# Kernel tuning notes

Hardware: AMD Instinct MI355X
Metric: run time of the kernel (lower is better)

The kernel has to match this reference:

```python
import jax, jax.numpy as jnp
import numpy as np
from jax import lax

V, E, H = 10000, 512, 512
B, L, T = 128, 8, 48


def setup_inputs() -> dict:
    key = jax.random.key(0)
    ks = jax.random.split(key, 12)
    s = lambda k, shape: jax.random.normal(k, shape, jnp.float32) * 0.05
    kw_lens = jnp.sort(jax.random.randint(ks[2], (B,), 1, L + 1))[::-1]  # descending, as pack_padded requires
    return {
        "kws": jax.random.randint(ks[0], (B, L), 0, V),
        "poem": jax.random.randint(ks[1], (B, T), 0, V),
        "kw_lens": kw_lens,
        "embedding": s(ks[3], (V, E)),
        "enc_Wih": s(ks[4], (4 * H, E)), "enc_Whh": s(ks[5], (4 * H, H)), "enc_b": s(ks[6], (4 * H,)),
        "dec_Wih": s(ks[7], (4 * H, E)), "dec_Whh": s(ks[8], (4 * H, H)), "dec_b": s(ks[9], (4 * H,)),
        "out_W": s(ks[10], (V, 2 * H)), "out_b": s(ks[11], (V,)),
    }


def _lstm_step(h, c, x, Wih, Whh, b):
    # PyTorch gate order: i, f, g, o
    gates = x @ Wih.T + h @ Whh.T + b  # [B, 4H]
    i, f, g, o = jnp.split(gates, 4, axis=-1)
    c = jax.nn.sigmoid(f) * c + jax.nn.sigmoid(i) * jnp.tanh(g)
    h = jax.nn.sigmoid(o) * jnp.tanh(c)
    return h, c


def reference(kws, poem, kw_lens, embedding, enc_Wih, enc_Whh, enc_b,
              dec_Wih, dec_Whh, dec_b, out_W, out_b):
    bs = kws.shape[0]
    mask = jnp.arange(L)[None, :] < kw_lens[:, None]  # sequence_mask, [B, L]

    # ---- encoder LSTM over keywords (dropout inactive at eval) ----
    kws_emb = embedding[kws]  # [B, L, E]

    def enc_scan(carry, x):
        h, c = carry
        h, c = _lstm_step(h, c, x, enc_Wih, enc_Whh, enc_b)
        return (h, c), (h, c)

    z = jnp.zeros((bs, H), embedding.dtype)
    _, (hs, cs) = lax.scan(enc_scan, (z, z), kws_emb.transpose(1, 0, 2))  # [L, B, H]
    kws_rep = hs.transpose(1, 0, 2) * mask[..., None]  # pad_packed zeros past length
    # pack semantics: final hidden is the state at the last valid timestep
    bidx = jnp.arange(bs)
    h0 = hs[kw_lens - 1, bidx]
    c0 = cs[kw_lens - 1, bidx]

    # ---- greedy per-timestep decode with dot-product attention ----
    neg = jnp.asarray(-1e9, embedding.dtype)

    def dec_scan(carry, tok):
        h, c = carry
        x = embedding[tok]  # [B, E]
        h, c = _lstm_step(h, c, x, dec_Wih, dec_Whh, dec_b)
        scores = jnp.einsum('bh,blh->bl', h, kws_rep)
        attn = jax.nn.softmax(jnp.where(mask, scores, neg), axis=-1)
        ctx = jnp.einsum('bl,blh->bh', attn, kws_rep)
        logits = jnp.concatenate([h, ctx], axis=-1) @ out_W.T + out_b  # [B, V]
        return (h, c), logits

    _, preds = lax.scan(dec_scan, (h0, c0), poem.T)  # [T, B, V]
    return preds.transpose(1, 0, 2)  # [B, T, V]
```

## Files before the change

### kernel.cpp

```cpp
#include <hip/hip_runtime.h>
#include <hip/hip_bf16.h>

typedef __bf16 bf16;
typedef __attribute__((ext_vector_type(8))) __bf16 bf16x8;
typedef __attribute__((ext_vector_type(4))) __bf16 bf16x4;
typedef __attribute__((ext_vector_type(4))) float f32x4;

#define B_ 128
#define L_ 8
#define T_ 48
#define V_ 10000
#define NBLK_REC 32
#define NBLK_TOT 240
#define NW (NBLK_TOT - NBLK_REC)

__device__ __forceinline__ float sigf(float x) { return 1.f / (1.f + expf(-x)); }

__device__ __forceinline__ void gl_lds16(const bf16* g, bf16* l) {
  __builtin_amdgcn_global_load_lds(
      (const __attribute__((address_space(1))) unsigned int*)g,
      (__attribute__((address_space(3))) unsigned int*)l, 16, 0, 0);
}

__device__ __forceinline__ unsigned aload32(const void* p) {
  return __hip_atomic_load((unsigned*)p, __ATOMIC_RELAXED, __HIP_MEMORY_SCOPE_AGENT);
}
__device__ __forceinline__ void astore64(void* p, unsigned long long v) {
  __hip_atomic_store((unsigned long long*)p, v, __ATOMIC_RELAXED, __HIP_MEMORY_SCOPE_AGENT);
}
__device__ __forceinline__ float bflo(unsigned u) { return __uint_as_float(u << 16); }
__device__ __forceinline__ float bfhi(unsigned u) { return __uint_as_float(u & 0xffff0000u); }
__device__ __forceinline__ unsigned packbf(float lo, float hi) {
  bf16 a = (bf16)lo, b = (bf16)hi;
  unsigned short ua = __builtin_bit_cast(unsigned short, a);
  unsigned short ub = __builtin_bit_cast(unsigned short, b);
  return (unsigned)ua | ((unsigned)ub << 16);
}

__global__ void prep_kernel(
    const int* __restrict__ kws, const int* __restrict__ poem,
    const float* __restrict__ emb,
    const float* __restrict__ eWih, const float* __restrict__ eWhh,
    const float* __restrict__ dWih, const float* __restrict__ dWhh,
    const float* __restrict__ outW,
    bf16* __restrict__ WihE, bf16* __restrict__ WhhE,
    bf16* __restrict__ WihD, bf16* __restrict__ WhhD,
    bf16* __restrict__ outWb,
    bf16* __restrict__ Xenc, bf16* __restrict__ Xdec,
    unsigned* __restrict__ ctl)
{
  if (blockIdx.x == 0)
    for (int i = threadIdx.x; i < 8192; i += blockDim.x) ctl[i] = 0u;
  const long SW = 1048576;
  const long SOWP = 10354688;
  const long SXE = 524288;
  const long SXD = 3145728;
  const long total = 4 * SW + SOWP + SXE + SXD;
  for (long i = blockIdx.x * (long)blockDim.x + threadIdx.x; i < total;
       i += (long)gridDim.x * blockDim.x) {
    long j = i;
    if (j < SW) { WihE[j] = (bf16)eWih[j]; continue; } j -= SW;
    if (j < SW) { WhhE[j] = (bf16)eWhh[j]; continue; } j -= SW;
    if (j < SW) { WihD[j] = (bf16)dWih[j]; continue; } j -= SW;
    if (j < SW) { WhhD[j] = (bf16)dWhh[j]; continue; } j -= SW;
    if (j < SOWP) {
      long r = j >> 10;
      outWb[j] = (r < 10000) ? (bf16)outW[j] : (bf16)0.f;
      continue;
    } j -= SOWP;
    if (j < SXE) {
      int e = (int)(j & 511); int b = (int)((j >> 9) & 127); int l = (int)(j >> 16);
      int tok = kws[b * L_ + l];
      Xenc[j] = (bf16)emb[(long)tok * 512 + e];
      continue;
    } j -= SXE;
    {
      int e = (int)(j & 511); int b = (int)((j >> 9) & 127); int t = (int)(j >> 16);
      int tok = poem[b * T_ + t];
      Xdec[j] = (bf16)emb[(long)tok * 512 + e];
    }
  }
}

__global__ __launch_bounds__(256) void gemm_pre_kernel(
    const bf16* __restrict__ A, const bf16* __restrict__ Bm,
    const float* __restrict__ bias, bf16* __restrict__ outp,
    int M, int N, int K, int MT)
{
  __shared__ bf16 As[128 * 32];
  __shared__ bf16 Bs[128 * 32];
  const int tid = threadIdx.x, lane = tid & 63, wid = tid >> 6;
  const int nwg = gridDim.x;
  int bid = blockIdx.x;
  int swz = ((nwg & 7) == 0) ? ((bid & 7) * (nwg >> 3) + (bid >> 3)) : bid;
  const int tm = swz % MT, tn = swz / MT;
  const int m0 = tm * 128, n0 = tn * 128;
  const int wm = (wid >> 1) * 64, wn = (wid & 1) * 64;
  const int fr = lane & 15, ku = lane >> 4;

  f32x4 acc[4][4];
  #pragma unroll
  for (int mi = 0; mi < 4; ++mi)
    #pragma unroll
    for (int ni = 0; ni < 4; ++ni) {
      acc[mi][ni][0] = 0.f; acc[mi][ni][1] = 0.f;
      acc[mi][ni][2] = 0.f; acc[mi][ni][3] = 0.f;
    }

  for (int kt = 0; kt < K; kt += 32) {
    #pragma unroll
    for (int j = 0; j < 2; ++j) {
      int i0 = j * 256 + wid * 64;
      int i = i0 + lane;
      int r = i >> 2, ub = i & 3;
      gl_lds16(A + (size_t)(m0 + r) * K + kt + ub * 8, As + (size_t)i0 * 8);
      gl_lds16(Bm + (size_t)(n0 + r) * K + kt + ub * 8, Bs + (size_t)i0 * 8);
    }
    __syncthreads();
    bf16x8 af[4], bfr[4];
    #pragma unroll
    for (int mi = 0; mi < 4; ++mi)
      af[mi] = *(const bf16x8*)(As + (size_t)(wm + mi * 16 + fr) * 32 + ku * 8);
    #pragma unroll
    for (int ni = 0; ni < 4; ++ni)
      bfr[ni] = *(const bf16x8*)(Bs + (size_t)(wn + ni * 16 + fr) * 32 + ku * 8);
    #pragma unroll
    for (int mi = 0; mi < 4; ++mi)
      #pragma unroll
      for (int ni = 0; ni < 4; ++ni)
        acc[mi][ni] = __builtin_amdgcn_mfma_f32_16x16x32_bf16(af[mi], bfr[ni], acc[mi][ni], 0, 0, 0);
    __syncthreads();
  }

  const int fq = (lane >> 4) * 4;
  #pragma unroll
  for (int mi = 0; mi < 4; ++mi) {
    #pragma unroll
    for (int ni = 0; ni < 4; ++ni) {
      #pragma unroll
      for (int j = 0; j < 4; ++j) {
        int r = m0 + wm + mi * 16 + fq + j;
        int cix = n0 + wn + ni * 16 + fr;
        outp[((size_t)(r >> 7) * 2048 + cix) * 128 + (r & 127)] = (bf16)(acc[mi][ni][j] + bias[cix]);
      }
    }
  }
}

__global__ __launch_bounds__(256, 1) void fused_kernel(
    const bf16* __restrict__ preEncT, bf16* __restrict__ preDecT,
    const bf16* __restrict__ WhhE, const bf16* __restrict__ WhhD,
    const int* __restrict__ kwl,
    bf16* __restrict__ hS, bf16* __restrict__ h0b,
    bf16* __restrict__ hsEnc, bf16* __restrict__ Hcat,
    const bf16* __restrict__ Xdec, const bf16* __restrict__ WihD,
    const float* __restrict__ db, const bf16* __restrict__ outWb,
    const float* __restrict__ outb, float* __restrict__ out,
    unsigned* __restrict__ ctl)
{
  __shared__ __align__(16) char pool[131072];
  const int tid = threadIdx.x, lane = tid & 63, wid = tid >> 6;

  if (blockIdx.x < NBLK_REC) {
    bf16* Bs = (bf16*)pool;
    bf16* As = (bf16*)(pool + 65536);
    unsigned* flg = ctl;
    const int blk = blockIdx.x, n0 = blk * 16;
    const int fr = lane & 15, fq = (lane >> 4) * 4, ku = lane >> 4;
    const int axor = fr & 7;
    const int arow0 = wid * 32 + fr, arow1 = wid * 32 + 16 + fr;
    const int row0 = wid * 32 + fq, row1 = wid * 32 + 16 + fq;
    const int brow = tid >> 1, bhalf = tid & 1;
    const int blen = kwl[brow];
    const int batt = blk * 4 + wid;
    const int lenb = kwl[batt];
    int lenr[2][4];
    #pragma unroll
    for (int j = 0; j < 4; ++j) { lenr[0][j] = kwl[row0 + j]; lenr[1][j] = kwl[row1 + j]; }

    auto signal = [&](unsigned step) {
      asm volatile("s_waitcnt vmcnt(0)" ::: "memory");
      __syncthreads();
      if (tid == 0)
        __hip_atomic_store(flg + blk * 32, step, __ATOMIC_RELAXED, __HIP_MEMORY_SCOPE_AGENT);
    };
    auto waitstep = [&](unsigned step) {
      if (tid < 64) {
        int l = tid;
        for (;;) {
          unsigned v = (l < NBLK_REC) ? aload32(flg + l * 32) : step;
          if (__all((int)(v >= step))) break;
          __builtin_amdgcn_s_sleep(1);
        }
      }
      __syncthreads();
    };

    auto loadB = [&](const bf16* W) {
      #pragma unroll
      for (int j = 0; j < 16; ++j) {
        int i = j * 256 + tid;
        int r = i >> 6, u = i & 63;
        int p = u ^ (r & 7);
        bf16x8 v = *(const bf16x8*)(W + (size_t)((r >> 4) * 512 + n0 + (r & 15)) * 512 + u * 8);
        *(bf16x8*)(Bs + (size_t)r * 512 + p * 8) = v;
      }
    };

    f32x4 acc[2][4];
    auto zacc = [&]() {
      #pragma unroll
      for (int mi = 0; mi < 2; ++mi)
        #pragma unroll
        for (int g = 0; g < 4; ++g) {
          acc[mi][g][0] = 0.f; acc[mi][g][1] = 0.f;
          acc[mi][g][2] = 0.f; acc[mi][g][3] = 0.f;
        }
    };

    auto gemm_full = [&](const bf16* h_in) {
      #pragma unroll
      for (int ch = 0; ch < 2; ++ch) {
        f32x4 tv[16];
        #pragma unroll
        for (int j = 0; j < 16; ++j) {
          int i = j * 256 + tid;
          int r = i >> 5, up = i & 31;
          const bf16* ga = h_in + (size_t)r * 512 + ch * 256 + up * 8;
          asm volatile("global_load_dwordx4 %0, %1, off sc0 sc1"
                       : "=v"(tv[j]) : "v"(ga) : "memory");
        }
        asm volatile("s_waitcnt vmcnt(0)" ::: "memory");
        __builtin_amdgcn_sched_barrier(0);
        #pragma unroll
        for (int j = 0; j < 16; ++j) {
          int i = j * 256 + tid;
          int r = i >> 5, up = i & 31;
          int s = up ^ (r & 7);
          *(f32x4*)(As + ((size_t)r * 32 + s) * 8) = tv[j];
        }
        __syncthreads();
        #pragma unroll
        for (int kt = 0; kt < 8; ++kt) {
          int cA = (kt * 4 + ku) ^ axor;
          int cB = ((ch * 8 + kt) * 4 + ku) ^ axor;
          bf16x8 af0 = *(const bf16x8*)(As + (size_t)arow0 * 256 + cA * 8);
          bf16x8 af1 = *(const bf16x8*)(As + (size_t)arow1 * 256 + cA * 8);
          #pragma unroll
          for (int g = 0; g < 4; ++g) {
            bf16x8 bv = *(const bf16x8*)(Bs + (size_t)(g * 16 + fr) * 512 + cB * 8);
            acc[0][g] = __builtin_amdgcn_mfma_f32_16x16x32_bf16(af0, bv, acc[0][g], 0, 0, 0);
            acc[1][g] = __builtin_amdgcn_mfma_f32_16x16x32_bf16(af1, bv, acc[1][g], 0, 0, 0);
          }
        }
        __syncthreads();
      }
    };

    float cr[2][4] = {{0.f,0.f,0.f,0.f},{0.f,0.f,0.f,0.f}};
    float c0r[2][4] = {{0.f,0.f,0.f,0.f},{0.f,0.f,0.f,0.f}};
    bf16 hout[2][4];
    bf16x4 gv[2][4];

    auto prefg = [&](const bf16* preT) {
      #pragma unroll
      for (int mi = 0; mi < 2; ++mi) {
        int rbase = mi ? row1 : row0;
        int hcol = n0 + fr;
        #pragma unroll
        for (int g = 0; g < 4; ++g)
          gv[mi][g] = *(const bf16x4*)(preT + ((size_t)(g * 512 + hcol)) * 128 + rbase);
      }
    };
    auto prefg_c = [&](const bf16* preT) {
      #pragma unroll
      for (int mi = 0; mi < 2; ++mi) {
        int rbase = mi ? row1 : row0;
        int hcol = n0 + fr;
        #pragma unroll
        for (int g = 0; g < 4; ++g) {
          const bf16* p = preT + ((size_t)(g * 512 + hcol)) * 128 + rbase;
          unsigned long long u;
          asm volatile("global_load_dwordx2 %0, %1, off sc0 sc1" : "=v"(u) : "v"(p) : "memory");
          gv[mi][g] = __builtin_bit_cast(bf16x4, u);
        }
      }
    };

    auto pointwise = [&]() {
      #pragma unroll
      for (int mi = 0; mi < 2; ++mi) {
        #pragma unroll
        for (int j = 0; j < 4; ++j) {
          float gi = acc[mi][0][j] + (float)gv[mi][0][j];
          float gf = acc[mi][1][j] + (float)gv[mi][1][j];
          float gg = acc[mi][2][j] + (float)gv[mi][2][j];
          float go = acc[mi][3][j] + (float)gv[mi][3][j];
          float cn = sigf(gf) * cr[mi][j] + sigf(gi) * tanhf(gg);
          float hn = sigf(go) * tanhf(cn);
          cr[mi][j] = cn;
          hout[mi][j] = (bf16)hn;
        }
      }
    };

    auto bounce_store = [&](bf16* hdst, bf16* hsdst, int t, int is_enc) {
      #pragma unroll
      for (int mi = 0; mi < 2; ++mi) {
        int rbase = mi ? row1 : row0;
        #pragma unroll
        for (int j = 0; j < 4; ++j)
          As[(size_t)(rbase + j) * 16 + fr] = hout[mi][j];
      }
      __syncthreads();
      unsigned long long v0 = *(unsigned long long*)(As + (size_t)brow * 16 + bhalf * 8);
      unsigned long long v1 = *(unsigned long long*)(As + (size_t)brow * 16 + bhalf * 8 + 4);
      size_t off = (size_t)brow * 512 + n0 + bhalf * 8;
      astore64(hdst + off, v0);
      astore64(hdst + off + 4, v1);
      if (is_enc) {
        unsigned long long m0 = (t < blen) ? v0 : 0ull;
        unsigned long long m1 = (t < blen) ? v1 : 0ull;
        astore64(hsdst + off, m0);
        astore64(hsdst + off + 4, m1);
        if (t == blen - 1) {
          astore64(h0b + off, v0);
          astore64(h0b + off + 4, v1);
        }
      }
    };

    unsigned hatt[4];
    auto load_hatt = [&](const bf16* h_in) {
      #pragma unroll
      for (int e = 0; e < 4; ++e) {
        const bf16* p = h_in + (size_t)batt * 512 + lane * 2 + 128 * e;
        asm volatile("global_load_dword %0, %1, off sc0 sc1" : "=v"(hatt[e]) : "v"(p) : "memory");
      }
    };

    unsigned hsr[8][4];

    auto attention = [&](int tprev) {
      asm volatile("s_waitcnt vmcnt(0)" ::: "memory");
      __builtin_amdgcn_sched_barrier(0);
      float sc[8];
      #pragma unroll
      for (int l = 0; l < 8; ++l) {
        float p = 0.f;
        #pragma unroll
        for (int e = 0; e < 4; ++e)
          p += bflo(hatt[e]) * bflo(hsr[l][e]) + bfhi(hatt[e]) * bfhi(hsr[l][e]);
        #pragma unroll
        for (int off = 32; off; off >>= 1) p += __shfl_xor(p, off);
        sc[l] = p;
      }
      float m = -1e30f;
      #pragma unroll
      for (int l = 0; l < 8; ++l) m = fmaxf(m, (l < lenb) ? sc[l] : -1e30f);
      float wgt[8]; float den = 0.f;
      #pragma unroll
      for (int l = 0; l < 8; ++l) { wgt[l] = (l < lenb) ? expf(sc[l] - m) : 0.f; den += wgt[l]; }
      float inv = 1.f / den;
      bf16* dst = Hcat + ((size_t)tprev * 128 + batt) * 1024;
      #pragma unroll
      for (int e = 0; e < 4; ++e) {
        float clo = 0.f, chi = 0.f;
        #pragma unroll
        for (int l = 0; l < 8; ++l) {
          clo += wgt[l] * bflo(hsr[l][e]);
          chi += wgt[l] * bfhi(hsr[l][e]);
        }
        unsigned cw = packbf(clo * inv, chi * inv);
        unsigned* d1 = (unsigned*)(dst + 512 + lane * 2 + 128 * e);
        unsigned* d0 = (unsigned*)(dst + lane * 2 + 128 * e);
        asm volatile("global_store_dword %0, %1, off sc0 sc1" :: "v"(d1), "v"(cw) : "memory");
        asm volatile("global_store_dword %0, %1, off sc0 sc1" :: "v"(d0), "v"(hatt[e]) : "memory");
      }
    };

    auto hcat_done = [&](int t) {
      asm volatile("s_waitcnt vmcnt(0)" ::: "memory");
      __syncthreads();
      if (tid == 0)
        __hip_atomic_fetch_add(ctl + 1056 + t * 32, 1u, __ATOMIC_RELAXED, __HIP_MEMORY_SCOPE_AGENT);
    };

    loadB(WhhE);
    __syncthreads();
    for (int t = 0; t < 8; ++t) {
      prefg(preEncT + (size_t)t * 262144);
      zacc();
      if (t > 0) {
        waitstep((unsigned)t);
        gemm_full(hS + (size_t)(t - 1) * 65536);
      }
      pointwise();
      #pragma unroll
      for (int mi = 0; mi < 2; ++mi)
        #pragma unroll
        for (int j = 0; j < 4; ++j)
          if (t == lenr[mi][j] - 1) c0r[mi][j] = cr[mi][j];
      bounce_store(hS + (size_t)t * 65536, hsEnc + (size_t)t * 65536, t, 1);
      signal((unsigned)(t + 1));
    }

    __syncthreads();
    loadB(WhhD);
    __syncthreads();
    waitstep(8u);
    #pragma unroll
    for (int l = 0; l < 8; ++l)
      #pragma unroll
      for (int e = 0; e < 4; ++e)
        hsr[l][e] = aload32(hsEnc + ((size_t)l * 128 + batt) * 512 + lane * 2 + 128 * e);
    #pragma unroll
    for (int mi = 0; mi < 2; ++mi)
      #pragma unroll
      for (int j = 0; j < 4; ++j) cr[mi][j] = c0r[mi][j];
    if (tid == 0) {
      unsigned v; int it = 0;
      do {
        asm volatile("global_load_dword %0, %1, off sc0 sc1\ns_waitcnt vmcnt(0)"
                     : "=v"(v) : "v"(ctl + 1024) : "memory");
        if (v >= 768u) break;
        __builtin_amdgcn_s_sleep(4);
      } while (++it < (1 << 20));
    }
    __syncthreads();

    for (int t = 0; t < 48; ++t) {
      prefg_c(preDecT + (size_t)t * 262144);
      zacc();
      const bf16* hin = (t == 0) ? (const bf16*)h0b
                                 : (const bf16*)(hS + (size_t)(8 + t - 1) * 65536);
      waitstep((unsigned)(8 + t));
      gemm_full(hin);
      pointwise();
      bounce_store(hS + (size_t)(8 + t) * 65536, nullptr, t, 0);
      signal((unsigned)(9 + t));
      if (t >= 1) {
        load_hatt(hin);
        attention(t - 1);
        hcat_done(t - 1);
      }
    }
    waitstep(56u);
    load_hatt(hS + (size_t)55 * 65536);
    attention(47);
    hcat_done(47);

  } else {
    bf16* AsW = (bf16*)pool;
    bf16* BsW = (bf16*)(pool + 8192);
    bf16* Tb  = (bf16*)(pool + 16384);
    const int w = blockIdx.x - NBLK_REC;
    const int fr = lane & 15, ku = lane >> 4;
    const int wm = (wid >> 1) * 64, wn = (wid & 1) * 64;
    const int fq = (lane >> 4) * 4;

    f32x4 acc[4][4];
    auto zacc = [&]() {
      #pragma unroll
      for (int mi = 0; mi < 4; ++mi)
        #pragma unroll
        for (int ni = 0; ni < 4; ++ni) {
          acc[mi][ni][0] = 0.f; acc[mi][ni][1] = 0.f;
          acc[mi][ni][2] = 0.f; acc[mi][ni][3] = 0.f;
        }
    };
    auto mfma_iter = [&]() {
      bf16x8 af[4], bfr[4];
      #pragma unroll
      for (int mi = 0; mi < 4; ++mi)
        af[mi] = *(const bf16x8*)(AsW + (size_t)(wm + mi * 16 + fr) * 32 + ku * 8);
      #pragma unroll
      for (int ni = 0; ni < 4; ++ni)
        bfr[ni] = *(const bf16x8*)(BsW + (size_t)(wn + ni * 16 + fr) * 32 + ku * 8);
      #pragma unroll
      for (int mi = 0; mi < 4; ++mi)
        #pragma unroll
        for (int ni = 0; ni < 4; ++ni)
          acc[mi][ni] = __builtin_amdgcn_mfma_f32_16x16x32_bf16(af[mi], bfr[ni], acc[mi][ni], 0, 0, 0);
    };
    auto wait_ge = [&](unsigned* p, unsigned target) {
      if (tid == 0) {
        unsigned v; int it = 0;
        do {
          asm volatile("global_load_dword %0, %1, off sc0 sc1\ns_waitcnt vmcnt(0)"
                       : "=v"(v) : "v"(p) : "memory");
          if (v >= target) break;
          __builtin_amdgcn_s_sleep(8);
        } while (++it < (1 << 20));
      }
      __syncthreads();
    };

    for (int i = w; i < 768; i += NW) {
      int t = i >> 4, tn = i & 15;
      int m0 = t * 128, n0 = tn * 128;
      zacc();
      for (int kt = 0; kt < 512; kt += 32) {
        #pragma unroll
        for (int j = 0; j < 2; ++j) {
          int i0 = j * 256 + wid * 64;
          int ii = i0 + lane;
          int r = ii >> 2, q = ii & 3;
          gl_lds16(Xdec + (size_t)(m0 + r) * 512 + kt + q * 8, AsW + (size_t)i0 * 8);
          gl_lds16(WihD + (size_t)(n0 + r) * 512 + kt + q * 8, BsW + (size_t)i0 * 8);
        }
        __syncthreads();
        mfma_iter();
        __syncthreads();
      }
      #pragma unroll
      for (int mi = 0; mi < 4; ++mi)
        #pragma unroll
        for (int ni = 0; ni < 4; ++ni) {
          int cl = wn + ni * 16 + fr;
          float bias = db[n0 + cl];
          #pragma unroll
          for (int j = 0; j < 4; ++j)
            Tb[(size_t)cl * 128 + (wm + mi * 16 + fq + j)] = (bf16)(acc[mi][ni][j] + bias);
        }
      __syncthreads();
      #pragma unroll
      for (int rep = 0; rep < 8; ++rep) {
        int u = rep * 256 + tid;
        int cl = u >> 4, cb = u & 15;
        f32x4 v = *(f32x4*)(Tb + (size_t)cl * 128 + cb * 8);
        bf16* dst = preDecT + ((size_t)t * 2048 + n0 + cl) * 128 + cb * 8;
        asm volatile("global_store_dwordx4 %0, %1, off sc0 sc1" :: "v"(dst), "v"(v) : "memory");
      }
      asm volatile("s_waitcnt vmcnt(0)" ::: "memory");
      __syncthreads();
      if (tid == 0)
        __hip_atomic_fetch_add(ctl + 1024, 1u, __ATOMIC_RELAXED, __HIP_MEMORY_SCOPE_AGENT);
      __syncthreads();
    }

    int seen = -1;
    for (int i = w; i < 3792; i += NW) {
      int t = i / 79, n = i % 79;
      if (t > seen) { wait_ge(ctl + 1056 + t * 32, (unsigned)NBLK_REC); seen = t; }
      int n0 = n * 128;
      zacc();
      for (int kt = 0; kt < 1024; kt += 32) {
        f32x4 v0, v1;
        {
          int u = tid, r = u >> 2, q = u & 3;
          const bf16* pa = Hcat + ((size_t)t * 128 + r) * 1024 + kt + q * 8;
          asm volatile("global_load_dwordx4 %0, %1, off sc0 sc1" : "=v"(v0) : "v"(pa) : "memory");
        }
        {
          int u = tid + 256, r = u >> 2, q = u & 3;
          const bf16* pa = Hcat + ((size_t)t * 128 + r) * 1024 + kt + q * 8;
          asm volatile("global_load_dwordx4 %0, %1, off sc0 sc1" : "=v"(v1) : "v"(pa) : "memory");
        }
        #pragma unroll
        for (int j = 0; j < 2; ++j) {
          int i0 = j * 256 + wid * 64;
          int ii = i0 + lane;
          int r = ii >> 2, q = ii & 3;
          gl_lds16(outWb + (size_t)(n0 + r) * 1024 + kt + q * 8, BsW + (size_t)i0 * 8);
        }
        asm volatile("s_waitcnt vmcnt(0)" ::: "memory");
        __builtin_amdgcn_sched_barrier(0);
        *(f32x4*)(AsW + (size_t)tid * 8) = v0;
        *(f32x4*)(AsW + ((size_t)tid + 256) * 8) = v1;
        __syncthreads();
        mfma_iter();
        __syncthreads();
      }
      #pragma unroll
      for (int mi = 0; mi < 4; ++mi) {
        #pragma unroll
        for (int ni = 0; ni < 4; ++ni) {
          int cix = n0 + wn + ni * 16 + fr;
          if (cix < V_) {
            float bias = outb[cix];
            #pragma unroll
            for (int j = 0; j < 4; ++j) {
              int b = wm + mi * 16 + fq + j;
              out[(size_t)b * (T_ * V_) + (size_t)t * V_ + cix] = acc[mi][ni][j] + bias;
            }
          }
        }
      }
    }
  }
}

extern "C" void kernel_launch(void* const* d_in, const int* in_sizes, int n_in,
                              void* d_out, int out_size, void* d_ws, size_t ws_size,
                              hipStream_t stream)
{
  const int* kws  = (const int*)d_in[0];
  const int* poem = (const int*)d_in[1];
  const int* kwl  = (const int*)d_in[2];
  const float* emb  = (const float*)d_in[3];
  const float* eWih = (const float*)d_in[4];
  const float* eWhh = (const float*)d_in[5];
  const float* eb   = (const float*)d_in[6];
  const float* dWih = (const float*)d_in[7];
  const float* dWhh = (const float*)d_in[8];
  const float* db   = (const float*)d_in[9];
  const float* outW = (const float*)d_in[10];
  const float* outb = (const float*)d_in[11];
  float* out = (float*)d_out;

  char* base = (char*)d_ws;
  size_t o = 0;
  auto take = [&](size_t bytes) -> char* {
    char* r = base + o;
    o += (bytes + 255) & ~(size_t)255;
    return r;
  };
  bf16* WihE  = (bf16*)take(2048 * 512 * 2);
  bf16* WhhE  = (bf16*)take(2048 * 512 * 2);
  bf16* WihD  = (bf16*)take(2048 * 512 * 2);
  bf16* WhhD  = (bf16*)take(2048 * 512 * 2);
  bf16* outWb = (bf16*)take((size_t)10112 * 1024 * 2);
  bf16* Xenc  = (bf16*)take(1024 * 512 * 2);
  bf16* Xdec  = (bf16*)take((size_t)6144 * 512 * 2);
  bf16* preEncT = (bf16*)take((size_t)8 * 2048 * 128 * 2);
  bf16* preDecT = (bf16*)take((size_t)48 * 2048 * 128 * 2);
  bf16* Hcat   = (bf16*)take((size_t)6144 * 1024 * 2);
  bf16* hS     = (bf16*)take((size_t)56 * 65536 * 2);
  bf16* hsEnc  = (bf16*)take((size_t)8 * 128 * 512 * 2);
  bf16* h0b    = (bf16*)take(128 * 512 * 2);
  unsigned* ctl = (unsigned*)take(32768);

  prep_kernel<<<4096, 256, 0, stream>>>(kws, poem, emb, eWih, eWhh, dWih, dWhh, outW,
                                        WihE, WhhE, WihD, WhhD, outWb, Xenc, Xdec, ctl);

  gemm_pre_kernel<<<128, 256, 0, stream>>>(Xenc, WihE, eb, preEncT, 1024, 2048, 512, 8);

  fused_kernel<<<NBLK_TOT, 256, 0, stream>>>(preEncT, preDecT, WhhE, WhhD, kwl,
                                             hS, h0b, hsEnc, Hcat,
                                             Xdec, WihD, db, outWb, outb, out, ctl);
}
```

Before: 720.4 us.

## Overlap recurrent h loads with MFMA and stream output-GEMM A tiles via LDS DMA

The recurrent gate GEMM now issues the global loads for the second K-chunk of h before running the MFMAs on the first chunk, so that load latency overlaps compute on the serial critical path. The per-step pre-activation gate reads switch from cache-bypassing inline-asm loads to ordinary loads. In the vocabulary projection GEMM, the activation tile is loaded with global_load_lds directly into LDS instead of passing through registers. These changes rely on ordinary cached loads and __syncthreads ordering to see data written by other blocks, which is a coherence risk, and the double-buffered registers add register pressure.

After: 739.0 us. 1.03x slower.

```diff
diff --git a/kernel.cpp b/kernel.cpp
--- a/kernel.cpp
+++ b/kernel.cpp
@@ -218,43 +218,72 @@
         }
     };
 
+    auto mfma_chunk = [&](int ch) {
+      #pragma unroll
+      for (int kt = 0; kt < 8; ++kt) {
+        int cA = (kt * 4 + ku) ^ axor;
+        int cB = ((ch * 8 + kt) * 4 + ku) ^ axor;
+        bf16x8 af0 = *(const bf16x8*)(As + (size_t)arow0 * 256 + cA * 8);
+        bf16x8 af1 = *(const bf16x8*)(As + (size_t)arow1 * 256 + cA * 8);
+        #pragma unroll
+        for (int g = 0; g < 4; ++g) {
+          bf16x8 bv = *(const bf16x8*)(Bs + (size_t)(g * 16 + fr) * 512 + cB * 8);
+          acc[0][g] = __builtin_amdgcn_mfma_f32_16x16x32_bf16(af0, bv, acc[0][g], 0, 0, 0);
+          acc[1][g] = __builtin_amdgcn_mfma_f32_16x16x32_bf16(af1, bv, acc[1][g], 0, 0, 0);
+        }
+      }
+    };
+
     auto gemm_full = [&](const bf16* h_in) {
-      #pragma unroll
-      for (int ch = 0; ch < 2; ++ch) {
-        f32x4 tv[16];
-        #pragma unroll
-        for (int j = 0; j < 16; ++j) {
-          int i = j * 256 + tid;
-          int r = i >> 5, up = i & 31;
-          const bf16* ga = h_in + (size_t)r * 512 + ch * 256 + up * 8;
-          asm volatile("global_load_dwordx4 %0, %1, off sc0 sc1"
-                       : "=v"(tv[j]) : "v"(ga) : "memory");
-        }
-        asm volatile("s_waitcnt vmcnt(0)" ::: "memory");
-        __builtin_amdgcn_sched_barrier(0);
-        #pragma unroll
-        for (int j = 0; j < 16; ++j) {
-          int i = j * 256 + tid;
-          int r = i >> 5, up = i & 31;
-          int s = up ^ (r & 7);
-          *(f32x4*)(As + ((size_t)r * 32 + s) * 8) = tv[j];
-        }
-        __syncthreads();
-        #pragma unroll
-        for (int kt = 0; kt < 8; ++kt) {
-          int cA = (kt * 4 + ku) ^ axor;
-          int cB = ((ch * 8 + kt) * 4 + ku) ^ axor;
-          bf16x8 af0 = *(const bf16x8*)(As + (size_t)arow0 * 256 + cA * 8);
-          bf16x8 af1 = *(const bf16x8*)(As + (size_t)arow1 * 256 + cA * 8);
-          #pragma unroll
-          for (int g = 0; g < 4; ++g) {
-            bf16x8 bv = *(const bf16x8*)(Bs + (size_t)(g * 16 + fr) * 512 + cB * 8);
-            acc[0][g] = __builtin_amdgcn_mfma_f32_16x16x32_bf16(af0, bv, acc[0][g], 0, 0, 0);
-            acc[1][g] = __builtin_amdgcn_mfma_f32_16x16x32_bf16(af1, bv, acc[1][g], 0, 0, 0);
-          }
-        }
-        __syncthreads();
-      }
+      f32x4 tv0[16], tv1[16];
+      #pragma unroll
+      for (int j = 0; j < 16; ++j) {
+        int i = j * 256 + tid;
+        int r = i >> 5, up = i & 31;
+        const bf16* ga = h_in + (size_t)r * 512 + up * 8;
+        asm volatile("global_load_dwordx4 %0, %1, off sc0 sc1"
+                     : "=v"(tv0[j]) : "v"(ga) : "memory");
+      }
+      asm volatile("s_waitcnt vmcnt(0)" ::: "memory");
+      __builtin_amdgcn_sched_barrier(0);
+      #pragma unroll
+      for (int j = 0; j < 16; ++j) {
+        int i = j * 256 + tid;
+        int r = i >> 5, up = i & 31;
+        int s = up ^ (r & 7);
+        *(f32x4*)(As + ((size_t)r * 32 + s) * 8) = tv0[j];
+      }
+      #pragma unroll
+      for (int j = 0; j < 16; ++j) {
+        int i = j * 256 + tid;
+        int r = i >> 5, up = i & 31;
+        const bf16* ga = h_in + (size_t)r * 512 + 256 + up * 8;
+        asm volatile("global_load_dwordx4 %0, %1, off sc0 sc1"
+                     : "=v"(tv1[j]) : "v"(ga) : "memory");
+      }
+      asm volatile("s_waitcnt lgkmcnt(0)" ::: "memory");
+      __builtin_amdgcn_sched_barrier(0);
+      __builtin_amdgcn_s_barrier();
+      mfma_chunk(0);
+      asm volatile("s_waitcnt lgkmcnt(0)" ::: "memory");
+      __builtin_amdgcn_sched_barrier(0);
+      __builtin_amdgcn_s_barrier();
+      asm volatile("s_waitcnt vmcnt(0)" ::: "memory");
+      __builtin_amdgcn_sched_barrier(0);
+      #pragma unroll
+      for (int j = 0; j < 16; ++j) {
+        int i = j * 256 + tid;
+        int r = i >> 5, up = i & 31;
+        int s = up ^ (r & 7);
+        *(f32x4*)(As + ((size_t)r * 32 + s) * 8) = tv1[j];
+      }
+      asm volatile("s_waitcnt lgkmcnt(0)" ::: "memory");
+      __builtin_amdgcn_sched_barrier(0);
+      __builtin_amdgcn_s_barrier();
+      mfma_chunk(1);
+      asm volatile("s_waitcnt lgkmcnt(0)" ::: "memory");
+      __builtin_amdgcn_sched_barrier(0);
+      __builtin_amdgcn_s_barrier();
     };
 
     float cr[2][4] = {{0.f,0.f,0.f,0.f},{0.f,0.f,0.f,0.f}};
@@ -270,20 +299,6 @@
         #pragma unroll
         for (int g = 0; g < 4; ++g)
           gv[mi][g] = *(const bf16x4*)(preT + ((size_t)(g * 512 + hcol)) * 128 + rbase);
-      }
-    };
-    auto prefg_c = [&](const bf16* preT) {
-      #pragma unroll
-      for (int mi = 0; mi < 2; ++mi) {
-        int rbase = mi ? row1 : row0;
-        int hcol = n0 + fr;
-        #pragma unroll
-        for (int g = 0; g < 4; ++g) {
-          const bf16* p = preT + ((size_t)(g * 512 + hcol)) * 128 + rbase;
-          unsigned long long u;
-          asm volatile("global_load_dwordx2 %0, %1, off sc0 sc1" : "=v"(u) : "v"(p) : "memory");
-          gv[mi][g] = __builtin_bit_cast(bf16x4, u);
-        }
       }
     };
 
@@ -430,7 +445,7 @@
     __syncthreads();
 
     for (int t = 0; t < 48; ++t) {
-      prefg_c(preDecT + (size_t)t * 262144);
+      prefg(preDecT + (size_t)t * 262144);
       zacc();
       const bf16* hin = (t == 0) ? (const bf16*)h0b
                                  : (const bf16*)(hS + (size_t)(8 + t - 1) * 65536);
@@ -544,30 +559,17 @@
       int t = i / 79, n = i % 79;
       if (t > seen) { wait_ge(ctl + 1056 + t * 32, (unsigned)NBLK_REC); seen = t; }
       int n0 = n * 128;
+      const bf16* Abase = Hcat + (size_t)t * 128 * 1024;
       zacc();
       for (int kt = 0; kt < 1024; kt += 32) {
-        f32x4 v0, v1;
-        {
-          int u = tid, r = u >> 2, q = u & 3;
-          const bf16* pa = Hcat + ((size_t)t * 128 + r) * 1024 + kt + q * 8;
-          asm volatile("global_load_dwordx4 %0, %1, off sc0 sc1" : "=v"(v0) : "v"(pa) : "memory");
-        }
-        {
-          int u = tid + 256, r = u >> 2, q = u & 3;
-          const bf16* pa = Hcat + ((size_t)t * 128 + r) * 1024 + kt + q * 8;
-          asm volatile("global_load_dwordx4 %0, %1, off sc0 sc1" : "=v"(v1) : "v"(pa) : "memory");
-        }
         #pragma unroll
         for (int j = 0; j < 2; ++j) {
           int i0 = j * 256 + wid * 64;
           int ii = i0 + lane;
           int r = ii >> 2, q = ii & 3;
+          gl_lds16(Abase + (size_t)r * 1024 + kt + q * 8, AsW + (size_t)i0 * 8);
           gl_lds16(outWb + (size_t)(n0 + r) * 1024 + kt + q * 8, BsW + (size_t)i0 * 8);
         }
-        asm volatile("s_waitcnt vmcnt(0)" ::: "memory");
-        __builtin_amdgcn_sched_barrier(0);
-        *(f32x4*)(AsW + (size_t)tid * 8) = v0;
-        *(f32x4*)(AsW + ((size_t)tid + 256) * 8) = v1;
         __syncthreads();
         mfma_iter();
         __syncthreads();
```

## Split attention into dedicated blocks and keep output weights resident in LDS

Applied to the files above, without the earlier changes.

Attention is moved off the recurrent LSTM blocks into 16 dedicated blocks that poll the per-step flags, so the recurrence critical path no longer carries the attention work. Each output-projection block now owns a fixed 64-column slice of out_W held in LDS for all 48 steps, reading the Hcat activations straight from global memory instead of restaging both operands every k-tile. The recurrent blocks also drop the cache-bypassing preDecT loads. The cost is fewer blocks for the projection (158 active), plain global reads of A without LDS staging, and another layer of flag synchronisation.

New measurement: 1.212 ms. 1.68x slower.

```diff
diff --git a/kernel.cpp b/kernel.cpp
--- a/kernel.cpp
+++ b/kernel.cpp
@@ -11,8 +11,9 @@
 #define T_ 48
 #define V_ 10000
 #define NBLK_REC 32
+#define NBLK_ATT 16
 #define NBLK_TOT 240
-#define NW (NBLK_TOT - NBLK_REC)
+#define NWG 192
 
 __device__ __forceinline__ float sigf(float x) { return 1.f / (1.f + expf(-x)); }
 
@@ -160,11 +161,23 @@
 {
   __shared__ __align__(16) char pool[131072];
   const int tid = threadIdx.x, lane = tid & 63, wid = tid >> 6;
+  unsigned* flg = ctl;
+
+  auto waitflags = [&](unsigned step) {
+    if (tid < 64) {
+      int l = tid;
+      for (;;) {
+        unsigned v = (l < NBLK_REC) ? aload32(flg + l * 32) : step;
+        if (__all((int)(v >= step))) break;
+        __builtin_amdgcn_s_sleep(1);
+      }
+    }
+    __syncthreads();
+  };
 
   if (blockIdx.x < NBLK_REC) {
     bf16* Bs = (bf16*)pool;
     bf16* As = (bf16*)(pool + 65536);
-    unsigned* flg = ctl;
     const int blk = blockIdx.x, n0 = blk * 16;
     const int fr = lane & 15, fq = (lane >> 4) * 4, ku = lane >> 4;
     const int axor = fr & 7;
@@ -172,8 +185,6 @@
     const int row0 = wid * 32 + fq, row1 = wid * 32 + 16 + fq;
     const int brow = tid >> 1, bhalf = tid & 1;
     const int blen = kwl[brow];
-    const int batt = blk * 4 + wid;
-    const int lenb = kwl[batt];
     int lenr[2][4];
     #pragma unroll
     for (int j = 0; j < 4; ++j) { lenr[0][j] = kwl[row0 + j]; lenr[1][j] = kwl[row1 + j]; }
@@ -183,17 +194,6 @@
       __syncthreads();
       if (tid == 0)
         __hip_atomic_store(flg + blk * 32, step, __ATOMIC_RELAXED, __HIP_MEMORY_SCOPE_AGENT);
-    };
-    auto waitstep = [&](unsigned step) {
-      if (tid < 64) {
-        int l = tid;
-        for (;;) {
-          unsigned v = (l < NBLK_REC) ? aload32(flg + l * 32) : step;
-          if (__all((int)(v >= step))) break;
-          __builtin_amdgcn_s_sleep(1);
-        }
-      }
-      __syncthreads();
     };
 
     auto loadB = [&](const bf16* W) {
@@ -270,20 +270,6 @@
         #pragma unroll
         for (int g = 0; g < 4; ++g)
           gv[mi][g] = *(const bf16x4*)(preT + ((size_t)(g * 512 + hcol)) * 128 + rbase);
-      }
-    };
-    auto prefg_c = [&](const bf16* preT) {
-      #pragma unroll
-      for (int mi = 0; mi < 2; ++mi) {
-        int rbase = mi ? row1 : row0;
-        int hcol = n0 + fr;
-        #pragma unroll
-        for (int g = 0; g < 4; ++g) {
-          const bf16* p = preT + ((size_t)(g * 512 + hcol)) * 128 + rbase;
-          unsigned long long u;
-          asm volatile("global_load_dwordx2 %0, %1, off sc0 sc1" : "=v"(u) : "v"(p) : "memory");
-          gv[mi][g] = __builtin_bit_cast(bf16x4, u);
-        }
       }
     };
 
@@ -330,69 +316,13 @@
       }
     };
 
-    unsigned hatt[4];
-    auto load_hatt = [&](const bf16* h_in) {
-      #pragma unroll
-      for (int e = 0; e < 4; ++e) {
-        const bf16* p = h_in + (size_t)batt * 512 + lane * 2 + 128 * e;
-        asm volatile("global_load_dword %0, %1, off sc0 sc1" : "=v"(hatt[e]) : "v"(p) : "memory");
-      }
-    };
-
-    unsigned hsr[8][4];
-
-    auto attention = [&](int tprev) {
-      asm volatile("s_waitcnt vmcnt(0)" ::: "memory");
-      __builtin_amdgcn_sched_barrier(0);
-      float sc[8];
-      #pragma unroll
-      for (int l = 0; l < 8; ++l) {
-        float p = 0.f;
-        #pragma unroll
-        for (int e = 0; e < 4; ++e)
-          p += bflo(hatt[e]) * bflo(hsr[l][e]) + bfhi(hatt[e]) * bfhi(hsr[l][e]);
-        #pragma unroll
-        for (int off = 32; off; off >>= 1) p += __shfl_xor(p, off);
-        sc[l] = p;
-      }
-      float m = -1e30f;
-      #pragma unroll
-      for (int l = 0; l < 8; ++l) m = fmaxf(m, (l < lenb) ? sc[l] : -1e30f);
-      float wgt[8]; float den = 0.f;
-      #pragma unroll
-      for (int l = 0; l < 8; ++l) { wgt[l] = (l < lenb) ? expf(sc[l] - m) : 0.f; den += wgt[l]; }
-      float inv = 1.f / den;
-      bf16* dst = Hcat + ((size_t)tprev * 128 + batt) * 1024;
-      #pragma unroll
-      for (int e = 0; e < 4; ++e) {
-        float clo = 0.f, chi = 0.f;
-        #pragma unroll
-        for (int l = 0; l < 8; ++l) {
-          clo += wgt[l] * bflo(hsr[l][e]);
-          chi += wgt[l] * bfhi(hsr[l][e]);
-        }
-        unsigned cw = packbf(clo * inv, chi * inv);
-        unsigned* d1 = (unsigned*)(dst + 512 + lane * 2 + 128 * e);
-        unsigned* d0 = (unsigned*)(dst + lane * 2 + 128 * e);
-        asm volatile("global_store_dword %0, %1, off sc0 sc1" :: "v"(d1), "v"(cw) : "memory");
-        asm volatile("global_store_dword %0, %1, off sc0 sc1" :: "v"(d0), "v"(hatt[e]) : "memory");
-      }
-    };
-
-    auto hcat_done = [&](int t) {
-      asm volatile("s_waitcnt vmcnt(0)" ::: "memory");
-      __syncthreads();
-      if (tid == 0)
-        __hip_atomic_fetch_add(ctl + 1056 + t * 32, 1u, __ATOMIC_RELAXED, __HIP_MEMORY_SCOPE_AGENT);
-    };
-
     loadB(WhhE);
     __syncthreads();
     for (int t = 0; t < 8; ++t) {
       prefg(preEncT + (size_t)t * 262144);
       zacc();
       if (t > 0) {
-        waitstep((unsigned)t);
+        waitflags((unsigned)t);
         gemm_full(hS + (size_t)(t - 1) * 65536);
       }
       pointwise();
@@ -408,12 +338,7 @@
     __syncthreads();
     loadB(WhhD);
     __syncthreads();
-    waitstep(8u);
-    #pragma unroll
-    for (int l = 0; l < 8; ++l)
-      #pragma unroll
-      for (int e = 0; e < 4; ++e)
-        hsr[l][e] = aload32(hsEnc + ((size_t)l * 128 + batt) * 512 + lane * 2 + 128 * e);
+    waitflags(8u);
     #pragma unroll
     for (int mi = 0; mi < 2; ++mi)
       #pragma unroll
@@ -430,59 +355,99 @@
     __syncthreads();
 
     for (int t = 0; t < 48; ++t) {
-      prefg_c(preDecT + (size_t)t * 262144);
+      prefg(preDecT + (size_t)t * 262144);
       zacc();
       const bf16* hin = (t == 0) ? (const bf16*)h0b
                                  : (const bf16*)(hS + (size_t)(8 + t - 1) * 65536);
-      waitstep((unsigned)(8 + t));
+      waitflags((unsigned)(8 + t));
       gemm_full(hin);
       pointwise();
       bounce_store(hS + (size_t)(8 + t) * 65536, nullptr, t, 0);
       signal((unsigned)(9 + t));
-      if (t >= 1) {
-        load_hatt(hin);
-        attention(t - 1);
-        hcat_done(t - 1);
-      }
-    }
-    waitstep(56u);
-    load_hatt(hS + (size_t)55 * 65536);
-    attention(47);
-    hcat_done(47);
+    }
+
+  } else if (blockIdx.x < NBLK_REC + NBLK_ATT) {
+    const int a = blockIdx.x - NBLK_REC;
+    const int b0 = a * 8 + wid * 2;
+    const int lenb0 = kwl[b0], lenb1 = kwl[b0 + 1];
+
+    waitflags(8u);
+    unsigned hsr[2][8][4];
+    #pragma unroll
+    for (int bb = 0; bb < 2; ++bb)
+      #pragma unroll
+      for (int l = 0; l < 8; ++l)
+        #pragma unroll
+        for (int e = 0; e < 4; ++e) {
+          const bf16* p = hsEnc + (size_t)l * 65536 + (size_t)(b0 + bb) * 512 + lane * 2 + 128 * e;
+          asm volatile("global_load_dword %0, %1, off sc0 sc1" : "=v"(hsr[bb][l][e]) : "v"(p) : "memory");
+        }
+    asm volatile("s_waitcnt vmcnt(0)" ::: "memory");
+    __builtin_amdgcn_sched_barrier(0);
+
+    for (int tp = 0; tp < 48; ++tp) {
+      waitflags((unsigned)(9 + tp));
+      const bf16* hin = hS + (size_t)(8 + tp) * 65536;
+      unsigned hatt[2][4];
+      #pragma unroll
+      for (int bb = 0; bb < 2; ++bb)
+        #pragma unroll
+        for (int e = 0; e < 4; ++e) {
+          const bf16* p = hin + (size_t)(b0 + bb) * 512 + lane * 2 + 128 * e;
+          asm volatile("global_load_dword %0, %1, off sc0 sc1" : "=v"(hatt[bb][e]) : "v"(p) : "memory");
+        }
+      asm volatile("s_waitcnt vmcnt(0)" ::: "memory");
+      __builtin_amdgcn_sched_barrier(0);
+      #pragma unroll
+      for (int bb = 0; bb < 2; ++bb) {
+        const int b = b0 + bb;
+        const int len = bb ? lenb1 : lenb0;
+        float sc[8];
+        #pragma unroll
+        for (int l = 0; l < 8; ++l) {
+          float p = 0.f;
+          #pragma unroll
+          for (int e = 0; e < 4; ++e)
+            p += bflo(hatt[bb][e]) * bflo(hsr[bb][l][e]) + bfhi(hatt[bb][e]) * bfhi(hsr[bb][l][e]);
+          #pragma unroll
+          for (int off = 32; off; off >>= 1) p += __shfl_xor(p, off);
+          sc[l] = p;
+        }
+        float m = -1e30f;
+        #pragma unroll
+        for (int l = 0; l < 8; ++l) m = fmaxf(m, (l < len) ? sc[l] : -1e30f);
+        float wgt[8]; float den = 0.f;
+        #pragma unroll
+        for (int l = 0; l < 8; ++l) { wgt[l] = (l < len) ? expf(sc[l] - m) : 0.f; den += wgt[l]; }
+        float inv = 1.f / den;
+        bf16* dst = Hcat + ((size_t)tp * 128 + b) * 1024;
+        #pragma unroll
+        for (int e = 0; e < 4; ++e) {
+          float clo = 0.f, chi = 0.f;
+          #pragma unroll
+          for (int l = 0; l < 8; ++l) {
+            clo += wgt[l] * bflo(hsr[bb][l][e]);
+            chi += wgt[l] * bfhi(hsr[bb][l][e]);
+          }
+          unsigned cw = packbf(clo * inv, chi * inv);
+          unsigned* d1 = (unsigned*)(dst + 512 + lane * 2 + 128 * e);
+          unsigned* d0 = (unsigned*)(dst + lane * 2 + 128 * e);
+          asm volatile("global_store_dword %0, %1, off sc0 sc1" :: "v"(d1), "v"(cw) : "memory");
+          asm volatile("global_store_dword %0, %1, off sc0 sc1" :: "v"(d0), "v"(hatt[bb][e]) : "memory");
+        }
+      }
+      asm volatile("s_waitcnt vmcnt(0)" ::: "memory");
+      __syncthreads();
+      if (tid == 0)
+        __hip_atomic_fetch_add(ctl + 1056 + tp * 32, 1u, __ATOMIC_RELAXED, __HIP_MEMORY_SCOPE_AGENT);
+      __syncthreads();
+    }
 
   } else {
-    bf16* AsW = (bf16*)pool;
-    bf16* BsW = (bf16*)(pool + 8192);
-    bf16* Tb  = (bf16*)(pool + 16384);
-    const int w = blockIdx.x - NBLK_REC;
+    const int w2 = blockIdx.x - NBLK_REC - NBLK_ATT;
     const int fr = lane & 15, ku = lane >> 4;
-    const int wm = (wid >> 1) * 64, wn = (wid & 1) * 64;
     const int fq = (lane >> 4) * 4;
 
-    f32x4 acc[4][4];
-    auto zacc = [&]() {
-      #pragma unroll
-      for (int mi = 0; mi < 4; ++mi)
-        #pragma unroll
-        for (int ni = 0; ni < 4; ++ni) {
-          acc[mi][ni][0] = 0.f; acc[mi][ni][1] = 0.f;
-          acc[mi][ni][2] = 0.f; acc[mi][ni][3] = 0.f;
-        }
-    };
-    auto mfma_iter = [&]() {
-      bf16x8 af[4], bfr[4];
-      #pragma unroll
-      for (int mi = 0; mi < 4; ++mi)
-        af[mi] = *(const bf16x8*)(AsW + (size_t)(wm + mi * 16 + fr) * 32 + ku * 8);
-      #pragma unroll
-      for (int ni = 0; ni < 4; ++ni)
-        bfr[ni] = *(const bf16x8*)(BsW + (size_t)(wn + ni * 16 + fr) * 32 + ku * 8);
-      #pragma unroll
-      for (int mi = 0; mi < 4; ++mi)
-        #pragma unroll
-        for (int ni = 0; ni < 4; ++ni)
-          acc[mi][ni] = __builtin_amdgcn_mfma_f32_16x16x32_bf16(af[mi], bfr[ni], acc[mi][ni], 0, 0, 0);
-    };
     auto wait_ge = [&](unsigned* p, unsigned target) {
       if (tid == 0) {
         unsigned v; int it = 0;
@@ -496,92 +461,128 @@
       __syncthreads();
     };
 
-    for (int i = w; i < 768; i += NW) {
-      int t = i >> 4, tn = i & 15;
-      int m0 = t * 128, n0 = tn * 128;
-      zacc();
-      for (int kt = 0; kt < 512; kt += 32) {
-        #pragma unroll
-        for (int j = 0; j < 2; ++j) {
-          int i0 = j * 256 + wid * 64;
-          int ii = i0 + lane;
-          int r = ii >> 2, q = ii & 3;
-          gl_lds16(Xdec + (size_t)(m0 + r) * 512 + kt + q * 8, AsW + (size_t)i0 * 8);
-          gl_lds16(WihD + (size_t)(n0 + r) * 512 + kt + q * 8, BsW + (size_t)i0 * 8);
-        }
+    {
+      bf16* AsW = (bf16*)pool;
+      bf16* BsW = (bf16*)(pool + 8192);
+      bf16* Tb  = (bf16*)(pool + 16384);
+      const int wm = (wid >> 1) * 64, wn = (wid & 1) * 64;
+      for (int i = w2; i < 768; i += NWG) {
+        int t = i >> 4, tn = i & 15;
+        int m0 = t * 128, n0 = tn * 128;
+        f32x4 acc[4][4];
+        #pragma unroll
+        for (int mi = 0; mi < 4; ++mi)
+          #pragma unroll
+          for (int ni = 0; ni < 4; ++ni) {
+            acc[mi][ni][0] = 0.f; acc[mi][ni][1] = 0.f;
+            acc[mi][ni][2] = 0.f; acc[mi][ni][3] = 0.f;
+          }
+        for (int kt = 0; kt < 512; kt += 32) {
+          #pragma unroll
+          for (int j = 0; j < 2; ++j) {
+            int i0 = j * 256 + wid * 64;
+            int ii = i0 + lane;
+            int r = ii >> 2, q = ii & 3;
+            gl_lds16(Xdec + (size_t)(m0 + r) * 512 + kt + q * 8, AsW + (size_t)i0 * 8);
+            gl_lds16(WihD + (size_t)(n0 + r) * 512 + kt + q * 8, BsW + (size_t)i0 * 8);
+          }
+          __syncthreads();
+          bf16x8 af[4], bfr[4];
+          #pragma unroll
+          for (int mi = 0; mi < 4; ++mi)
+            af[mi] = *(const bf16x8*)(AsW + (size_t)(wm + mi * 16 + fr) * 32 + ku * 8);
+          #pragma unroll
+          for (int ni = 0; ni < 4; ++ni)
+            bfr[ni] = *(const bf16x8*)(BsW + (size_t)(wn + ni * 16 + fr) * 32 + ku * 8);
+          #pragma unroll
+          for (int mi = 0; mi < 4; ++mi)
+            #pragma unroll
+            for (int ni = 0; ni < 4; ++ni)
+              acc[mi][ni] = __builtin_amdgcn_mfma_f32_16x16x32_bf16(af[mi], bfr[ni], acc[mi][ni], 0, 0, 0);
+          __syncthreads();
+        }
+        #pragma unroll
+        for (int mi = 0; mi < 4; ++mi)
+          #pragma unroll
+          for (int ni = 0; ni < 4; ++ni) {
+            int cl = wn + ni * 16 + fr;
+            float bias = db[n0 + cl];
+            #pragma unroll
+            for (int j = 0; j < 4; ++j)
+              Tb[(size_t)cl * 128 + (wm + mi * 16 + fq + j)] = (bf16)(acc[mi][ni][j] + bias);
+          }
         __syncthreads();
-        mfma_iter();
+        #pragma unroll
+        for (int rep = 0; rep < 8; ++rep) {
+          int u = rep * 256 + tid;
+          int cl = u >> 4, cb = u & 15;
+          f32x4 v = *(f32x4*)(Tb + (size_t)cl * 128 + cb * 8);
+          bf16* dst = preDecT + ((size_t)t * 2048 + n0 + cl) * 128 + cb * 8;
+          asm volatile("global_store_dwordx4 %0, %1, off sc0 sc1" :: "v"(dst), "v"(v) : "memory");
+        }
+        asm volatile("s_waitcnt vmcnt(0)" ::: "memory");
         __syncthreads();
-      }
+        if (tid == 0)
+          __hip_atomic_fetch_add(ctl + 1024, 1u, __ATOMIC_RELAXED, __HIP_MEMORY_SCOPE_AGENT);
+        __syncthreads();
+      }
+    }
+
+    if (w2 >= 158) return;
+    const int n = w2 >> 1, half = w2 & 1;
+    const int ncol0 = n * 128 + half * 64;
+    bf16* Blds = (bf16*)pool;
+    __syncthreads();
+    for (int q = 0; q < 32; ++q) {
+      int i0 = q * 256 + wid * 64;
+      int i = i0 + lane;
+      int r = i >> 7, u = i & 127;
+      gl_lds16(outWb + (size_t)(ncol0 + r) * 1024 + (size_t)(u ^ (r & 7)) * 8,
+               Blds + (size_t)i0 * 8);
+    }
+    asm volatile("s_waitcnt vmcnt(0)" ::: "memory");
+    __syncthreads();
+
+    const int wm2 = (wid >> 1) * 64, wn2 = (wid & 1) * 32;
+    for (int t = 0; t < 48; ++t) {
+      wait_ge(ctl + 1056 + t * 32, (unsigned)NBLK_ATT);
+      const bf16* Abase = Hcat + (size_t)t * 131072;
+      f32x4 acc[4][2];
       #pragma unroll
       for (int mi = 0; mi < 4; ++mi)
         #pragma unroll
-        for (int ni = 0; ni < 4; ++ni) {
-          int cl = wn + ni * 16 + fr;
-          float bias = db[n0 + cl];
-          #pragma unroll
-          for (int j = 0; j < 4; ++j)
-            Tb[(size_t)cl * 128 + (wm + mi * 16 + fq + j)] = (bf16)(acc[mi][ni][j] + bias);
-        }
-      __syncthreads();
-      #pragma unroll
-      for (int rep = 0; rep < 8; ++rep) {
-        int u = rep * 256 + tid;
-        int cl = u >> 4, cb = u & 15;
-        f32x4 v = *(f32x4*)(Tb + (size_t)cl * 128 + cb * 8);
-        bf16* dst = preDecT + ((size_t)t * 2048 + n0 + cl) * 128 + cb * 8;
-        asm volatile("global_store_dwordx4 %0, %1, off sc0 sc1" :: "v"(dst), "v"(v) : "memory");
-      }
-      asm volatile("s_waitcnt vmcnt(0)" ::: "memory");
-      __syncthreads();
-      if (tid == 0)
-        __hip_atomic_fetch_add(ctl + 1024, 1u, __ATOMIC_RELAXED, __HIP_MEMORY_SCOPE_AGENT);
-      __syncthreads();
-    }
-
-    int seen = -1;
-    for (int i = w; i < 3792; i += NW) {
-      int t = i / 79, n = i % 79;
-      if (t > seen) { wait_ge(ctl + 1056 + t * 32, (unsigned)NBLK_REC); seen = t; }
-      int n0 = n * 128;
-      zacc();
+        for (int ni = 0; ni < 2; ++ni) {
+          acc[mi][ni][0] = 0.f; acc[mi][ni][1] = 0.f;
+          acc[mi][ni][2] = 0.f; acc[mi][ni][3] = 0.f;
+        }
+      #pragma unroll 4
       for (int kt = 0; kt < 1024; kt += 32) {
-        f32x4 v0, v1;
-        {
-          int u = tid, r = u >> 2, q = u & 3;
-          const bf16* pa = Hcat + ((size_t)t * 128 + r) * 1024 + kt + q * 8;
-          asm volatile("global_load_dwordx4 %0, %1, off sc0 sc1" : "=v"(v0) : "v"(pa) : "memory");
-        }
-        {
-          int u = tid + 256, r = u >> 2, q = u & 3;
-          const bf16* pa = Hcat + ((size_t)t * 128 + r) * 1024 + kt + q * 8;
-          asm volatile("global_load_dwordx4 %0, %1, off sc0 sc1" : "=v"(v1) : "v"(pa) : "memory");
-        }
-        #pragma unroll
-        for (int j = 0; j < 2; ++j) {
-          int i0 = j * 256 + wid * 64;
-          int ii = i0 + lane;
-          int r = ii >> 2, q = ii & 3;
-          gl_lds16(outWb + (size_t)(n0 + r) * 1024 + kt + q * 8, BsW + (size_t)i0 * 8);
-        }
-        asm volatile("s_waitcnt vmcnt(0)" ::: "memory");
-        __builtin_amdgcn_sched_barrier(0);
-        *(f32x4*)(AsW + (size_t)tid * 8) = v0;
-        *(f32x4*)(AsW + ((size_t)tid + 256) * 8) = v1;
-        __syncthreads();
-        mfma_iter();
-        __syncthreads();
+        bf16x8 af[4], bfv[2];
+        #pragma unroll
+        for (int mi = 0; mi < 4; ++mi)
+          af[mi] = *(const bf16x8*)(Abase + (size_t)(wm2 + mi * 16 + fr) * 1024 + kt + ku * 8);
+        int ukb = (kt >> 3) + ku;
+        #pragma unroll
+        for (int ni = 0; ni < 2; ++ni) {
+          int row = wn2 + ni * 16 + fr;
+          bfv[ni] = *(const bf16x8*)(Blds + ((size_t)row * 128 + (ukb ^ (row & 7))) * 8);
+        }
+        #pragma unroll
+        for (int mi = 0; mi < 4; ++mi)
+          #pragma unroll
+          for (int ni = 0; ni < 2; ++ni)
+            acc[mi][ni] = __builtin_amdgcn_mfma_f32_16x16x32_bf16(af[mi], bfv[ni], acc[mi][ni], 0, 0, 0);
       }
       #pragma unroll
       for (int mi = 0; mi < 4; ++mi) {
         #pragma unroll
-        for (int ni = 0; ni < 4; ++ni) {
-          int cix = n0 + wn + ni * 16 + fr;
+        for (int ni = 0; ni < 2; ++ni) {
+          int cix = ncol0 + wn2 + ni * 16 + fr;
           if (cix < V_) {
             float bias = outb[cix];
             #pragma unroll
             for (int j = 0; j < 4; ++j) {
-              int b = wm + mi * 16 + fq + j;
+              int b = wm2 + mi * 16 + fq + j;
               out[(size_t)b * (T_ * V_) + (size_t)t * V_ + cix] = acc[mi][ni][j] + bias;
             }
           }
```
